# Kernel tuning notes

Hardware: AMD Instinct MI355X
Metric: run time of the kernel (lower is better)

## Reference

```python
import jax, jax.numpy as jnp
import numpy as np
from jax import lax

N_KERNELS = 11
N_GRAMS = 3
EMB = 300
CONV_OUT = 128
B, QLEN, DLEN = 128, 30, 256


def _kernel_mus(n):
    mus = [1.0]
    bin_size = 2.0 / (n - 1)
    mus.append(1 - bin_size / 2)
    for i in range(1, n - 1):
        mus.append(mus[i] - bin_size)
    return mus


def _kernel_sigmas(n):
    bin_size = 2.0 / (n - 1)
    return [0.001] + [0.5 * bin_size] * (n - 1)


MU = jnp.asarray(np.array(_kernel_mus(N_KERNELS), dtype=np.float32))      # [K]
SIGMA = jnp.asarray(np.array(_kernel_sigmas(N_KERNELS), dtype=np.float32))  # [K]


def setup_inputs() -> dict:
    key = jax.random.key(0)
    ks = jax.random.split(key, 10)
    inp = {
        "query_embeddings": jax.random.normal(ks[0], (B, QLEN, EMB), jnp.float32),
        "document_embeddings": jax.random.normal(ks[1], (B, DLEN, EMB), jnp.float32),
        "query_pad_oov_mask": jnp.ones((B, QLEN), jnp.float32),
        "document_pad_oov_mask": jnp.ones((B, DLEN), jnp.float32),
    }
    # conv weights for n-gram sizes 1..3: [out_ch, in_ch, ksize]
    for i in range(1, N_GRAMS + 1):
        inp[f"conv_w{i}"] = jax.random.normal(ks[1 + i], (CONV_OUT, EMB, i), jnp.float32) * 0.05
        inp[f"conv_b{i}"] = jnp.zeros((CONV_OUT,), jnp.float32)
    inp["dense_w"] = jax.random.uniform(ks[9], (1, N_KERNELS * N_GRAMS * N_GRAMS), jnp.float32,
                                        minval=-0.014, maxval=0.014)
    return inp


def _conv_ngram(x, w, b):
    # x: [B, L, E]; w: [C, E, k]; right-pad by k-1 so output length == L (ConstantPad1d((0,k-1)))
    k = w.shape[-1]
    y = lax.conv_general_dilated(x.transpose(0, 2, 1), w, (1,), [(0, k - 1)],
                                 dimension_numbers=("NCH", "OIH", "NCH"))
    return jax.nn.relu(y + b[None, :, None]).transpose(0, 2, 1)  # [B, L, C]


def _kernel_pool(q, d, qd_mask, q_mask):
    # cosine matrix (AllenNLP CosineMatrixAttention: normalize with +1e-13 eps)
    qn = q / (jnp.linalg.norm(q, axis=-1, keepdims=True) + 1e-13)
    dn = d / (jnp.linalg.norm(d, axis=-1, keepdims=True) + 1e-13)
    cos = jnp.einsum("bqe,bde->bqd", qn, dn) * qd_mask  # [B, Q, D]
    # RBF soft-histogram kernels: [B, Q, D, K]
    k = jnp.exp(-(cos[..., None] - MU) ** 2 / (2.0 * SIGMA ** 2)) * qd_mask[..., None]
    per_kernel_query = k.sum(axis=2)  # [B, Q, K]
    log_pk = jnp.log(jnp.clip(per_kernel_query, 1e-10, None)) * 0.01
    return (log_pk * q_mask[..., None]).sum(axis=1)  # [B, K]


def reference(query_embeddings, document_embeddings, query_pad_oov_mask, document_pad_oov_mask,
              conv_w1, conv_b1, conv_w2, conv_b2, conv_w3, conv_b3, dense_w):
    qd_mask = query_pad_oov_mask[:, :, None] * document_pad_oov_mask[:, None, :]  # [B, Q, D]
    conv_params = [(conv_w1, conv_b1), (conv_w2, conv_b2), (conv_w3, conv_b3)]
    q_res = [_conv_ngram(query_embeddings, w, b) for w, b in conv_params]
    d_res = [_conv_ngram(document_embeddings, w, b) for w, b in conv_params]
    matched = [_kernel_pool(q_res[i], d_res[t], qd_mask, query_pad_oov_mask)
               for i in range(N_GRAMS) for t in range(N_GRAMS)]
    all_grams = jnp.concatenate(matched, axis=1)  # [B, K*9]
    return jnp.squeeze(all_grams @ dense_w.T, axis=1)  # [B]
```

## Files before the change

### kernel.cpp

```cpp
#include <hip/hip_runtime.h>
#include <math.h>


typedef __bf16 bf16x8 __attribute__((ext_vector_type(8)));
typedef float f32x4 __attribute__((ext_vector_type(4)));

#if __has_builtin(__builtin_amdgcn_exp2f)
#define EXP2F(x) __builtin_amdgcn_exp2f(x)
#else
#define EXP2F(x) exp2f(x)
#endif

#define AS_STRIDE 344

static __device__ __forceinline__ unsigned short f2bf(float f) {
  union { float f; unsigned int u; } v; v.f = f;
  unsigned int r = v.u + 0x7FFFu + ((v.u >> 16) & 1u);
  return (unsigned short)(r >> 16);
}

__global__ __launch_bounds__(256) void prep(
    const float* __restrict__ w1, const float* __restrict__ w2,
    const float* __restrict__ w3,
    const float* __restrict__ qemb, const float* __restrict__ demb,
    unsigned short* __restrict__ wt2,
    unsigned short* __restrict__ qx, unsigned short* __restrict__ dx) {
  const int bid = blockIdx.x;
  const int t = threadIdx.x;
  if (bid < 960) {
    int idx = bid * 256 + t;
    if (idx >= 245760) return;
    int jj   = idx & 7;
    int lane = (idx >> 3) & 63;
    int ec   = (idx >> 9) % 10;
    int cb   = (idx / 5120) & 7;
    int p    = idx / 40960;
    const float* w; int k, jt;
    if (p == 0)      { w = w1; k = 1; jt = 0; }
    else if (p <= 2) { w = w2; k = 2; jt = p - 1; }
    else             { w = w3; k = 3; jt = p - 3; }
    int c = cb * 16 + (lane & 15);
    int e = ec * 32 + (lane >> 4) * 8 + jj;
    float v = (e < 300) ? w[(c * 300 + e) * k + jt] : 0.0f;
    wt2[idx] = f2bf(v);
  } else {
    int idx = (bid - 960) * 256 + t;
    if (idx >= 1474560) return;
    int c8   = idx % 40;
    int ridx = idx / 40;
    const float* src; unsigned short* dst; int valid;
    if (ridx < 4096) {
      int b = ridx >> 5, r = ridx & 31;
      valid = (r < 30);
      src = qemb + ((size_t)b * 30 + r) * 300;
      dst = qx + (size_t)ridx * 320;
    } else {
      int rd = ridx - 4096;
      valid = 1;
      src = demb + (size_t)rd * 300;
      dst = dx + (size_t)rd * 320;
    }
    int e = c8 * 8;
    float4 a = make_float4(0.f, 0.f, 0.f, 0.f);
    float4 c = make_float4(0.f, 0.f, 0.f, 0.f);
    if (valid && e < 300)     a = *reinterpret_cast<const float4*>(src + e);
    if (valid && e + 4 < 300) c = *reinterpret_cast<const float4*>(src + e + 4);
    uint4 o;
    o.x = (unsigned int)f2bf(a.x) | ((unsigned int)f2bf(a.y) << 16);
    o.y = (unsigned int)f2bf(a.z) | ((unsigned int)f2bf(a.w) << 16);
    o.z = (unsigned int)f2bf(c.x) | ((unsigned int)f2bf(c.y) << 16);
    o.w = (unsigned int)f2bf(c.z) | ((unsigned int)f2bf(c.w) << 16);
    *reinterpret_cast<uint4*>(dst + e) = o;
  }
}

template<int NI>
__device__ __forceinline__ void conv_body(
    unsigned short* As, float* psq,
    const unsigned short* __restrict__ xs, int L, int Lpad, int l0, int b,
    const unsigned short* __restrict__ wt2,
    const float* __restrict__ b1, const float* __restrict__ b2,
    const float* __restrict__ b3,
    unsigned short* __restrict__ out) {
  constexpr int ROWS = NI * 16 + 2;
  constexpr int NR = NI * 16;
  const int t = threadIdx.x;
  const int w = __builtin_amdgcn_readfirstlane(t >> 6);
  const int lane = t & 63;
  const int quad = lane >> 4, lrow = lane & 15;

  for (int idx = t; idx < ROWS * 40; idx += 512) {
    int r = idx / 40, c = idx % 40;
    int l = l0 + r;
    uint4 v = make_uint4(0u, 0u, 0u, 0u);
    if (l < Lpad) v = *reinterpret_cast<const uint4*>(xs + (size_t)l * 320 + c * 8);
    *reinterpret_cast<uint4*>(&As[r * AS_STRIDE + c * 8]) = v;
  }
  __syncthreads();

  f32x4 acc[NI][3];
  #pragma unroll
  for (int ni = 0; ni < NI; ++ni)
    #pragma unroll
    for (int g = 0; g < 3; ++g) acc[ni][g] = (f32x4){0.f, 0.f, 0.f, 0.f};

  const unsigned short* wl = wt2 + (size_t)lane * 8;

  #pragma unroll 2
  for (int ec = 0; ec < 10; ++ec) {
    #pragma unroll
    for (int j = 0; j < 3; ++j) {
      bf16x8 xf[NI];
      #pragma unroll
      for (int ni = 0; ni < NI; ++ni)
        xf[ni] = *reinterpret_cast<const bf16x8*>(
            &As[(ni * 16 + lrow + j) * AS_STRIDE + ec * 32 + quad * 8]);
      #pragma unroll
      for (int g = j; g < 3; ++g) {
        const int pst = (g * (g + 1)) >> 1;
        bf16x8 wf = *reinterpret_cast<const bf16x8*>(
            wl + ((((pst + j) * 8 + w) * 10 + ec) << 9));
        #pragma unroll
        for (int ni = 0; ni < NI; ++ni)
          acc[ni][g] = __builtin_amdgcn_mfma_f32_16x16x32_bf16(
              wf, xf[ni], acc[ni][g], 0, 0, 0);
      }
    }
  }

  const float* biases[3] = {b1, b2, b3};
  float4 bv[3];
  #pragma unroll
  for (int g = 0; g < 3; ++g)
    bv[g] = *reinterpret_cast<const float4*>(biases[g] + w * 16 + quad * 4);

  #pragma unroll
  for (int ni = 0; ni < NI; ++ni) {
    #pragma unroll
    for (int g = 0; g < 3; ++g) {
      float p = 0.f;
      #pragma unroll
      for (int r = 0; r < 4; ++r) {
        float y = fmaxf(acc[ni][g][r] + bv[g][r], 0.f);
        p += y * y;
      }
      p += __shfl_xor(p, 16);
      p += __shfl_xor(p, 32);
      if (lane < 16) psq[(w * 3 + g) * NR + ni * 16 + lrow] = p;
    }
  }
  __syncthreads();

  #pragma unroll
  for (int ni = 0; ni < NI; ++ni) {
    int row = ni * 16 + lrow;
    int l = l0 + row;
    if (l < L) {
      #pragma unroll
      for (int g = 0; g < 3; ++g) {
        float ssq = 0.f;
        #pragma unroll
        for (int wv = 0; wv < 8; ++wv) ssq += psq[(wv * 3 + g) * NR + row];
        float inv = 1.0f / (sqrtf(ssq) + 1e-13f);
        unsigned int pk[2];
        #pragma unroll
        for (int h = 0; h < 2; ++h) {
          float y0 = fmaxf(acc[ni][g][2 * h + 0] + bv[g][2 * h + 0], 0.f) * inv;
          float y1 = fmaxf(acc[ni][g][2 * h + 1] + bv[g][2 * h + 1], 0.f) * inv;
          pk[h] = (unsigned int)f2bf(y0) | ((unsigned int)f2bf(y1) << 16);
        }
        unsigned short* op = out + ((size_t)(g * 128 + b) * L + l) * 128 +
                             w * 16 + quad * 4;
        *reinterpret_cast<uint2*>(op) = make_uint2(pk[0], pk[1]);
      }
    }
  }
}

__global__ __launch_bounds__(512, 4) void conv_all(
    const unsigned short* __restrict__ qx, const unsigned short* __restrict__ dx,
    const unsigned short* __restrict__ wt2,
    const float* __restrict__ b1, const float* __restrict__ b2,
    const float* __restrict__ b3,
    unsigned short* __restrict__ qn, unsigned short* __restrict__ dn) {
  __shared__ unsigned short As[66 * AS_STRIDE];
  __shared__ float psq[8 * 3 * 64];
  const int bi = blockIdx.x;
  if (bi < 512)
    conv_body<4>(As, psq, dx + (size_t)(bi >> 2) * 256 * 320, 256, 256,
                 (bi & 3) * 64, bi >> 2, wt2, b1, b2, b3, dn);
  else
    conv_body<2>(As, psq, qx + (size_t)(bi - 512) * 32 * 320, 30, 32,
                 0, bi - 512, wt2, b1, b2, b3, qn);
}

__global__ __launch_bounds__(64) void pool_mfma(
    const unsigned short* __restrict__ qn, const unsigned short* __restrict__ dn,
    const float* __restrict__ qmask, const float* __restrict__ dmask,
    float* __restrict__ pkq8) {
  const float A2[11] = {2.0f, 1.8f, 1.4f, 1.0f, 0.6f, 0.2f,
                        -0.2f, -0.6f, -1.0f, -1.4f, -1.8f};
  const float CC[11] = {-721347.52f, -58.429149f, -35.346028f, -18.033688f,
                        -6.4921277f, -0.72134752f, -0.72134752f, -6.4921277f,
                        -18.033688f, -35.346028f, -58.429149f};
  const int tg    = blockIdx.x >> 3;
  const int chunk = blockIdx.x & 7;
  const int b     = blockIdx.y;
  const int lane  = threadIdx.x;
  const int quad  = lane >> 4, l15 = lane & 15;
  const int d0    = chunk * 32;

  const unsigned short* dslab = dn + (size_t)(tg * 128 + b) * 256 * 128;

  bf16x8 aD[2][4];
  #pragma unroll
  for (int mi = 0; mi < 2; ++mi)
    #pragma unroll
    for (int kt = 0; kt < 4; ++kt)
      aD[mi][kt] = *reinterpret_cast<const bf16x8*>(
          dslab + (size_t)(d0 + mi * 16 + l15) * 128 + kt * 32 + quad * 8);

  float dmv[2][4];
  #pragma unroll
  for (int mi = 0; mi < 2; ++mi)
    #pragma unroll
    for (int r = 0; r < 4; ++r)
      dmv[mi][r] = dmask[b * 256 + d0 + mi * 16 + quad * 4 + r];

  float qmv[2];
  qmv[0] = qmask[b * 30 + l15];
  qmv[1] = (16 + l15 < 30) ? qmask[b * 30 + 16 + l15] : 0.0f;

  #pragma unroll 1
  for (int ig = 0; ig < 3; ++ig) {
    const unsigned short* qslab = qn + (size_t)(ig * 128 + b) * 30 * 128;

    bf16x8 bQ[2][4];
    #pragma unroll
    for (int ni = 0; ni < 2; ++ni)
      #pragma unroll
      for (int kt = 0; kt < 4; ++kt)
        bQ[ni][kt] = *reinterpret_cast<const bf16x8*>(
            qslab + (size_t)(ni * 16 + l15) * 128 + kt * 32 + quad * 8);

    f32x4 acc[2][2];
    #pragma unroll
    for (int mi = 0; mi < 2; ++mi)
      #pragma unroll
      for (int ni = 0; ni < 2; ++ni) acc[mi][ni] = (f32x4){0.f, 0.f, 0.f, 0.f};

    #pragma unroll
    for (int kt = 0; kt < 4; ++kt)
      #pragma unroll
      for (int mi = 0; mi < 2; ++mi)
        #pragma unroll
        for (int ni = 0; ni < 2; ++ni)
          acc[mi][ni] = __builtin_amdgcn_mfma_f32_16x16x32_bf16(
              aD[mi][kt], bQ[ni][kt], acc[mi][ni], 0, 0, 0);

    float feat[2][11];
    #pragma unroll
    for (int ni = 0; ni < 2; ++ni)
      #pragma unroll
      for (int kk = 0; kk < 11; ++kk) feat[ni][kk] = 0.0f;

    #pragma unroll
    for (int mi = 0; mi < 2; ++mi) {
      #pragma unroll
      for (int r = 0; r < 4; ++r) {
        #pragma unroll
        for (int ni = 0; ni < 2; ++ni) {
          float m  = qmv[ni] * dmv[mi][r];
          float cm = acc[mi][ni][r] * m;
          float w0 = cm * -721347.52f;
          float w1 = cm * -72.134752f;
          #pragma unroll
          for (int kk = 0; kk < 11; ++kk) {
            float wk = (kk == 0) ? w0 : w1;
            float e = EXP2F(fmaf(wk, cm - A2[kk], CC[kk]));
            feat[ni][kk] += e * m;
          }
        }
      }
    }

    #pragma unroll
    for (int ni = 0; ni < 2; ++ni)
      #pragma unroll
      for (int kk = 0; kk < 11; ++kk) {
        float v = feat[ni][kk];
        v += __shfl_xor(v, 16);
        v += __shfl_xor(v, 32);
        feat[ni][kk] = v;
      }

    if (quad == 0) {
      const int pair = ig * 3 + tg;
      #pragma unroll
      for (int ni = 0; ni < 2; ++ni) {
        int q = ni * 16 + l15;
        if (q < 30) {
          float* p = pkq8 +
              (((size_t)(chunk * 9 + pair) * 128 + b) * 30 + q) * 11;
          #pragma unroll
          for (int kk = 0; kk < 11; ++kk) p[kk] = feat[ni][kk];
        }
      }
    }
  }
}

__global__ __launch_bounds__(256) void final_kernel(
    const float* __restrict__ pkq8, const float* __restrict__ qmask,
    const float* __restrict__ dw, float* __restrict__ out) {
  const int CH = 9 * 128 * 30 * 11;
  const int b = blockIdx.x;
  const int t = threadIdx.x;
  float s = 0.0f;
  for (int idx = t; idx < 9 * 30 * 11; idx += 256) {
    int pair = idx / 330;
    int rem  = idx % 330;
    int q    = rem / 11;
    int kk   = rem % 11;
    size_t base = (((size_t)pair * 128 + b) * 30 + q) * 11 + kk;
    float v = 0.f;
    #pragma unroll
    for (int c = 0; c < 8; ++c) v += pkq8[base + (size_t)c * CH];
    s += __logf(fmaxf(v, 1e-10f)) * 0.01f * qmask[b * 30 + q] * dw[pair * 11 + kk];
  }
  s += __shfl_xor(s, 1);  s += __shfl_xor(s, 2);  s += __shfl_xor(s, 4);
  s += __shfl_xor(s, 8);  s += __shfl_xor(s, 16); s += __shfl_xor(s, 32);
  __shared__ float part[4];
  if ((t & 63) == 0) part[t >> 6] = s;
  __syncthreads();
  if (t == 0) out[b] = part[0] + part[1] + part[2] + part[3];
}

extern "C" void kernel_launch(void* const* d_in, const int* in_sizes, int n_in,
                              void* d_out, int out_size, void* d_ws, size_t ws_size,
                              hipStream_t stream) {
  const float* qemb  = (const float*)d_in[0];
  const float* demb  = (const float*)d_in[1];
  const float* qmask = (const float*)d_in[2];
  const float* dmask = (const float*)d_in[3];
  const float* w1 = (const float*)d_in[4];
  const float* b1 = (const float*)d_in[5];
  const float* w2 = (const float*)d_in[6];
  const float* b2 = (const float*)d_in[7];
  const float* w3 = (const float*)d_in[8];
  const float* b3 = (const float*)d_in[9];
  const float* dw = (const float*)d_in[10];

  unsigned short* ws  = (unsigned short*)d_ws;
  unsigned short* wt2 = ws;
  unsigned short* qx  = ws + 245760;
  unsigned short* dx  = ws + 1556480;
  unsigned short* qn  = ws + 12042240;
  unsigned short* dn  = ws + 13516800;
  float*          pkq8 = (float*)(ws + 245760);
  float* out = (float*)d_out;

  prep<<<6720, 256, 0, stream>>>(w1, w2, w3, qemb, demb, wt2, qx, dx);
  conv_all<<<640, 512, 0, stream>>>(qx, dx, wt2, b1, b2, b3, qn, dn);
  pool_mfma<<<dim3(24, 128), 64, 0, stream>>>(qn, dn, qmask, dmask, pkq8);
  final_kernel<<<128, 256, 0, stream>>>(pkq8, qmask, dw, out);
}
```

Before: 179.2 us.

## Double-buffer conv weight loads with inline asm and explicit vmcnt waits

Weight fragments for the n-gram conv MFMA loop are now fetched one embedding chunk ahead into two register buffers, using inline global_load_dwordx4 with manual s_waitcnt vmcnt and sched barriers. The first weight load is issued before the LDS barrier. The goal is to hide global-load latency behind the MFMA work of the previous chunk. In exchange it uses more registers and depends on the hand-counted vmcnt values being right; a miscount would read weights before they arrive.

```diff
diff --git a/kernel.cpp b/kernel.cpp
--- a/kernel.cpp
+++ b/kernel.cpp
@@ -96,36 +96,60 @@
     if (l < Lpad) v = *reinterpret_cast<const uint4*>(xs + (size_t)l * 320 + c * 8);
     *reinterpret_cast<uint4*>(&As[r * AS_STRIDE + c * 8]) = v;
   }
+
+  f32x4 acc[NI][3];
+  #pragma unroll
+  for (int ni = 0; ni < NI; ++ni)
+    #pragma unroll
+    for (int g = 0; g < 3; ++g) acc[ni][g] = (f32x4){0.f, 0.f, 0.f, 0.f};
+
+  const unsigned short* wl = wt2 + (size_t)lane * 8;
+
+  auto issue = [&](bf16x8* dst, int ec) {
+    #pragma unroll
+    for (int p = 0; p < 6; ++p) {
+      const unsigned short* a = wl + (size_t)((((p * 8 + w) * 10 + ec)) << 9);
+      asm volatile("global_load_dwordx4 %0, %1, off"
+                   : "=v"(dst[p]) : "v"(a));
+    }
+  };
+
+  auto compute = [&](const bf16x8* wf, int ec) {
+    bf16x8 xf[3][NI];
+    #pragma unroll
+    for (int j = 0; j < 3; ++j)
+      #pragma unroll
+      for (int ni = 0; ni < NI; ++ni)
+        xf[j][ni] = *reinterpret_cast<const bf16x8*>(
+            &As[(ni * 16 + lrow + j) * AS_STRIDE + ec * 32 + quad * 8]);
+    const int PJ[6] = {0, 0, 1, 0, 1, 2};
+    const int PG[6] = {0, 1, 1, 2, 2, 2};
+    #pragma unroll
+    for (int p = 0; p < 6; ++p)
+      #pragma unroll
+      for (int ni = 0; ni < NI; ++ni)
+        acc[ni][PG[p]] = __builtin_amdgcn_mfma_f32_16x16x32_bf16(
+            wf[p], xf[PJ[p]][ni], acc[ni][PG[p]], 0, 0, 0);
+  };
+
+  bf16x8 bufA[6], bufB[6];
+  issue(bufA, 0);
   __syncthreads();
 
-  f32x4 acc[NI][3];
-  #pragma unroll
-  for (int ni = 0; ni < NI; ++ni)
-    #pragma unroll
-    for (int g = 0; g < 3; ++g) acc[ni][g] = (f32x4){0.f, 0.f, 0.f, 0.f};
-
-  const unsigned short* wl = wt2 + (size_t)lane * 8;
-
-  #pragma unroll 2
-  for (int ec = 0; ec < 10; ++ec) {
-    #pragma unroll
-    for (int j = 0; j < 3; ++j) {
-      bf16x8 xf[NI];
-      #pragma unroll
-      for (int ni = 0; ni < NI; ++ni)
-        xf[ni] = *reinterpret_cast<const bf16x8*>(
-            &As[(ni * 16 + lrow + j) * AS_STRIDE + ec * 32 + quad * 8]);
-      #pragma unroll
-      for (int g = j; g < 3; ++g) {
-        const int pst = (g * (g + 1)) >> 1;
-        bf16x8 wf = *reinterpret_cast<const bf16x8*>(
-            wl + ((((pst + j) * 8 + w) * 10 + ec) << 9));
-        #pragma unroll
-        for (int ni = 0; ni < NI; ++ni)
-          acc[ni][g] = __builtin_amdgcn_mfma_f32_16x16x32_bf16(
-              wf, xf[ni], acc[ni][g], 0, 0, 0);
-      }
-    }
+  #pragma unroll
+  for (int ec = 0; ec < 10; ec += 2) {
+    issue(bufB, ec + 1);
+    asm volatile("s_waitcnt vmcnt(6)");
+    __builtin_amdgcn_sched_barrier(0);
+    compute(bufA, ec);
+    if (ec + 2 < 10) {
+      issue(bufA, ec + 2);
+      asm volatile("s_waitcnt vmcnt(6)");
+    } else {
+      asm volatile("s_waitcnt vmcnt(0)");
+    }
+    __builtin_amdgcn_sched_barrier(0);
+    compute(bufB, ec + 1);
   }
 
   const float* biases[3] = {b1, b2, b3};
```

Result: slower. 183.6 us (+2.5%).
